# Kernel tuning notes

Hardware: AMD Instinct MI355X
Metric: run time of the kernel (lower is better)

The kernel has to match this reference:

```python
import jax, jax.numpy as jnp
import numpy as np

MAX_NUM_BINS = 200
BIN_SIZE = 500
NUM_NEIGHBORS = 5
DIST_MULT = 0.1


def setup_inputs() -> dict:
    key = jax.random.key(0)
    k1, k2 = jax.random.split(key)
    points = jax.random.normal(k1, (2, 5000, 128), dtype=jnp.float32)
    rotations = jax.random.normal(k2, (128, MAX_NUM_BINS // 2), dtype=jnp.float32)
    return {"points": points, "rotations": rotations}


def reference(points, rotations):
    # points: [B, N, D], rotations: [D, max_num_bins//2]
    B, N, D = points.shape
    nbins = N // BIN_SIZE  # module requires N % BIN_SIZE == 0

    # LSH bin assignment: project onto nbins//2 random directions, sign-split into nbins bins
    mul = jnp.einsum('bnd,dh->bnh', points, rotations[:, :nbins // 2])  # [B,N,nbins//2]
    cmul = jnp.concatenate([mul, -mul], axis=-1)                        # [B,N,nbins]
    bin_idx = jnp.argmax(cmul, axis=-1)                                 # [B,N]
    # equal-size bins via argsort of bin id (matches tf argsort+reshape)
    bins_split = jnp.argsort(bin_idx, axis=-1).reshape(B, nbins, BIN_SIZE)  # [B,nbins,S]

    # gather points per bin
    parts = jnp.take_along_axis(points, bins_split.reshape(B, N, 1), axis=1)
    parts = parts.reshape(B, nbins, BIN_SIZE, D)

    # per-bin pairwise distance -> gaussian kernel
    na = jnp.sum(parts * parts, axis=-1)                                # [B,nbins,S]
    gram = jnp.einsum('bcid,bcjd->bcij', parts, parts)                  # [B,nbins,S,S]
    dist = jnp.sqrt(jnp.maximum(na[..., :, None] - 2.0 * gram + na[..., None, :], 1e-6))
    dm = jnp.exp(-DIST_MULT * dist)                                     # [B,nbins,S,S]

    # top-k neighbors within each bin
    vals, idx = jax.lax.top_k(dm, NUM_NEIGHBORS)                        # [B,nbins,S,K]

    # map local bin indices back to global point indices
    bs_flat = bins_split.reshape(B * nbins, BIN_SIZE)
    dst = jnp.take_along_axis(bs_flat, idx.reshape(B * nbins, BIN_SIZE * NUM_NEIGHBORS), axis=1)
    dst = dst.reshape(B, nbins, BIN_SIZE, NUM_NEIGHBORS)
    src = jnp.broadcast_to(bins_split[..., None], dst.shape)
    bidx = jnp.broadcast_to(jnp.arange(B)[:, None, None, None], dst.shape)

    # scatter-add into dense [B,N,N] (sparse.add sums duplicate entries)
    out = jnp.zeros((B, N, N), dtype=points.dtype)
    out = out.at[bidx.reshape(-1), src.reshape(-1), dst.reshape(-1)].add(vals.reshape(-1))
    return out
```

## Files before the change

### kernel.cpp

```cpp
#include <hip/hip_runtime.h>
#include <cfloat>
#include <math.h>

#define NPTS   5000
#define BATCH  2
#define DIM    128
#define NBINS  10
#define BINSZ  500
#define TOPK   5
#define ROTCOLS 100

#define KB_PTS 64
#define KB_STR 129
__global__ void k_bins(const float* __restrict__ pts, const float* __restrict__ rot,
                       int* __restrict__ bin_idx, double* __restrict__ na) {
    __shared__ float P[KB_PTS * KB_STR];
    __shared__ float rotL[DIM * 5];
    int tid = threadIdx.x;
    for (int f = tid; f < DIM * 5; f += 256)
        rotL[f] = rot[(f / 5) * ROTCOLS + (f % 5)];

    int p0  = blockIdx.x * KB_PTS;
    int npb = min(KB_PTS, BATCH * NPTS - p0);

    for (int f = tid; f < npb * DIM; f += 256) {
        int r = f >> 7, d = f & 127;
        P[r * KB_STR + d] = pts[(size_t)(p0 + r) * DIM + d];
    }
    __syncthreads();

    int p = tid >> 2;
    int s = tid & 3;
    double acc[5] = {0., 0., 0., 0., 0.};
    double sq = 0.;
    const float* row = &P[p * KB_STR + s * 32];
    for (int j = 0; j < 32; ++j) {
        double v = (double)row[j];
        sq += v * v;
        int d = s * 32 + j;
#pragma unroll
        for (int h = 0; h < 5; ++h) acc[h] += v * (double)rotL[d * 5 + h];
    }
#pragma unroll
    for (int m = 1; m < 4; m <<= 1) {
#pragma unroll
        for (int h = 0; h < 5; ++h) acc[h] += __shfl_xor(acc[h], m, 4);
        sq += __shfl_xor(sq, m, 4);
    }
    if (s == 0 && p < npb) {
        double best = acc[0]; int bc = 0;
#pragma unroll
        for (int c = 1; c < NBINS; ++c) {
            double v = (c < 5) ? acc[c] : -acc[c - 5];
            if (v > best) { best = v; bc = c; }
        }
        bin_idx[p0 + p] = bc;
        na[p0 + p] = sq;
    }
}

__global__ void k_sort(const int* __restrict__ bin_idx, int* __restrict__ order) {
    const int b = blockIdx.x;
    const int t = threadIdx.x;
    const int NPT = (NPTS + 255) / 256;
    int start = t * NPT;
    int end   = min(NPTS, start + NPT);

    int cnt[NBINS];
#pragma unroll
    for (int c = 0; c < NBINS; ++c) cnt[c] = 0;
    for (int i = start; i < end; ++i) {
        int c = bin_idx[b * NPTS + i];
#pragma unroll
        for (int k = 0; k < NBINS; ++k) cnt[k] += (c == k);
    }

    __shared__ int hist[NBINS * 256];
#pragma unroll
    for (int c = 0; c < NBINS; ++c) hist[c * 256 + t] = cnt[c];
    __syncthreads();

    int base = t * NBINS;
    int s = 0;
#pragma unroll
    for (int k = 0; k < NBINS; ++k) s += hist[base + k];
    __shared__ int scan[256];
    scan[t] = s;
    __syncthreads();
    for (int off = 1; off < 256; off <<= 1) {
        int v = (t >= off) ? scan[t - off] : 0;
        __syncthreads();
        scan[t] += v;
        __syncthreads();
    }
    int run = scan[t] - s;
#pragma unroll
    for (int k = 0; k < NBINS; ++k) { int h = hist[base + k]; hist[base + k] = run; run += h; }
    __syncthreads();

    int ofs[NBINS];
#pragma unroll
    for (int c = 0; c < NBINS; ++c) ofs[c] = hist[c * 256 + t];
    for (int i = start; i < end; ++i) {
        int c = bin_idx[b * NPTS + i];
        int pos = 0;
#pragma unroll
        for (int k = 0; k < NBINS; ++k) {
            if (c == k) pos = ofs[k];
            ofs[k] += (c == k);
        }
        order[b * NPTS + pos] = i;
    }
}

#define RT    16
#define NRT   32
#define CTILE 64
#define RSTRD 130
#define CSTR  132
#define NCT   8
#define ROWQ  (NPTS/4)

__launch_bounds__(256, 3)
__global__ void k_chunks(const float* __restrict__ pts, const double* __restrict__ na,
                         const int* __restrict__ order, float* __restrict__ out) {
    __shared__ double rowPd[RT * RSTRD];
    __shared__ float  colP[CTILE * CSTR];
    __shared__ double naC[CTILE];
    __shared__ double naRs[RT];
    __shared__ int    ordR[RT];

    int blk   = blockIdx.x;
    int rt    = blk & (NRT - 1);
    int chunk = blk >> 5;
    int b     = chunk / NBINS;
    int c     = chunk % NBINS;
    int tid   = threadIdx.x;
    int row0  = rt * RT;
    int rowCount = min(RT, BINSZ - row0);

    const int*   ordBase = order + b * NPTS + c * BINSZ;
    const float* ptsB    = pts + (size_t)b * NPTS * DIM;

    for (int f = tid; f < rowCount * (DIM / 4); f += 256) {
        int r = f >> 5;
        int q = f & 31;
        int g = ordBase[row0 + r];
        float4 v = *(const float4*)(ptsB + (size_t)g * DIM + q * 4);
        double2 d01; d01.x = (double)v.x; d01.y = (double)v.y;
        double2 d23; d23.x = (double)v.z; d23.y = (double)v.w;
        *(double2*)(&rowPd[r * RSTRD + q * 4 + 0]) = d01;
        *(double2*)(&rowPd[r * RSTRD + q * 4 + 2]) = d23;
    }
    if (tid < rowCount) {
        int g = ordBase[row0 + tid];
        ordR[tid] = g;
        naRs[tid] = na[b * NPTS + g];
    }
    __syncthreads();

    int cg  = tid & 15;
    int ks  = (tid >> 4) & 1;
    int rg  = tid >> 5;
    int cgm = tid & 31;
    const int q0 = ks * 64;

    double naRr0 = (rg     < rowCount) ? naRs[rg]     : 0.;
    double naRr1 = (rg + 8 < rowCount) ? naRs[rg + 8] : 0.;

    double tv[2][TOPK];
    int    tl[2][TOPK];
#pragma unroll
    for (int ii = 0; ii < 2; ++ii)
#pragma unroll
        for (int k = 0; k < TOPK; ++k) { tv[ii][k] = DBL_MAX; tl[ii][k] = 0x7fffffff; }

    const int totalZ = rowCount * ROWQ;

    for (int ct = 0; ct < NCT; ++ct) {
        int col0T = ct * CTILE;
        int colCount = min(CTILE, BINSZ - col0T);
        __syncthreads();
        for (int f = tid; f < colCount * (DIM / 4); f += 256) {
            int j = f >> 5;
            int q = f & 31;
            int g = ordBase[col0T + j];
            float4 v = *(const float4*)(ptsB + (size_t)g * DIM + q * 4);
            *(float4*)(&colP[j * CSTR + q * 4]) = v;
        }
        if (tid < colCount) {
            int g = ordBase[col0T + tid];
            naC[tid] = na[b * NPTS + g];
        }
        __syncthreads();

        {
            float4 z = make_float4(0.f, 0.f, 0.f, 0.f);
            int z0 = (ct * totalZ) / NCT, z1 = ((ct + 1) * totalZ) / NCT;
            for (int f = z0 + tid; f < z1; f += 256) {
                int r = f / ROWQ;
                int q = f - r * ROWQ;
                float* outRow = out + ((size_t)b * NPTS + ordR[r]) * NPTS;
                *(float4*)(outRow + 4 * q) = z;
            }
        }

        double acc00 = 0., acc01 = 0., acc02 = 0., acc03 = 0.;
        double acc10 = 0., acc11 = 0., acc12 = 0., acc13 = 0.;

        for (int q = 0; q < 64; q += 4) {
            const int qq = q0 + q;
            double2 a0lo = *(const double2*)(&rowPd[rg * RSTRD + qq + 0]);
            double2 a0hi = *(const double2*)(&rowPd[rg * RSTRD + qq + 2]);
            double2 a1lo = *(const double2*)(&rowPd[(rg + 8) * RSTRD + qq + 0]);
            double2 a1hi = *(const double2*)(&rowPd[(rg + 8) * RSTRD + qq + 2]);
            float4 f0 = *(const float4*)(&colP[cg * CSTR + qq]);
            float4 f1 = *(const float4*)(&colP[(cg + 16) * CSTR + qq]);
            float4 f2 = *(const float4*)(&colP[(cg + 32) * CSTR + qq]);
            float4 f3 = *(const float4*)(&colP[(cg + 48) * CSTR + qq]);
            double b0x = (double)f0.x, b0y = (double)f0.y, b0z = (double)f0.z, b0w = (double)f0.w;
            double b1x = (double)f1.x, b1y = (double)f1.y, b1z = (double)f1.z, b1w = (double)f1.w;
            double b2x = (double)f2.x, b2y = (double)f2.y, b2z = (double)f2.z, b2w = (double)f2.w;
            double b3x = (double)f3.x, b3y = (double)f3.y, b3z = (double)f3.z, b3w = (double)f3.w;
            acc00 += a0lo.x * b0x + a0lo.y * b0y + a0hi.x * b0z + a0hi.y * b0w;
            acc01 += a0lo.x * b1x + a0lo.y * b1y + a0hi.x * b1z + a0hi.y * b1w;
            acc02 += a0lo.x * b2x + a0lo.y * b2y + a0hi.x * b2z + a0hi.y * b2w;
            acc03 += a0lo.x * b3x + a0lo.y * b3y + a0hi.x * b3z + a0hi.y * b3w;
            acc10 += a1lo.x * b0x + a1lo.y * b0y + a1hi.x * b0z + a1hi.y * b0w;
            acc11 += a1lo.x * b1x + a1lo.y * b1y + a1hi.x * b1z + a1hi.y * b1w;
            acc12 += a1lo.x * b2x + a1lo.y * b2y + a1hi.x * b2z + a1hi.y * b2w;
            acc13 += a1lo.x * b3x + a1lo.y * b3y + a1hi.x * b3z + a1hi.y * b3w;
        }

        acc00 += __shfl_xor(acc00, 16, 64);
        acc01 += __shfl_xor(acc01, 16, 64);
        acc02 += __shfl_xor(acc02, 16, 64);
        acc03 += __shfl_xor(acc03, 16, 64);
        acc10 += __shfl_xor(acc10, 16, 64);
        acc11 += __shfl_xor(acc11, 16, 64);
        acc12 += __shfl_xor(acc12, 16, 64);
        acc13 += __shfl_xor(acc13, 16, 64);

        double selA0 = ks ? acc02 : acc00;
        double selA1 = ks ? acc12 : acc10;
        double selB0 = ks ? acc03 : acc01;
        double selB1 = ks ? acc13 : acc11;
        int colA = cg + (ks ? 32 : 0);
        int colB = cg + (ks ? 48 : 16);

        if (colA < colCount) {
            int    cl = col0T + colA;
            double nc = naC[colA];
            double cv0 = fmax(naRr0 + nc - 2. * selA0, 1e-6);
            double cv1 = fmax(naRr1 + nc - 2. * selA1, 1e-6);
            int cl0 = cl, cl1 = cl;
#pragma unroll
            for (int k = 0; k < TOPK; ++k) {
                bool lt0 = (cv0 < tv[0][k]);
                double ov0 = tv[0][k]; int ol0 = tl[0][k];
                if (lt0) { tv[0][k] = cv0; tl[0][k] = cl0; cv0 = ov0; cl0 = ol0; }
                bool lt1 = (cv1 < tv[1][k]);
                double ov1 = tv[1][k]; int ol1 = tl[1][k];
                if (lt1) { tv[1][k] = cv1; tl[1][k] = cl1; cv1 = ov1; cl1 = ol1; }
            }
        }
        if (colB < colCount) {
            int    cl = col0T + colB;
            double nc = naC[colB];
            double cv0 = fmax(naRr0 + nc - 2. * selB0, 1e-6);
            double cv1 = fmax(naRr1 + nc - 2. * selB1, 1e-6);
            int cl0 = cl, cl1 = cl;
#pragma unroll
            for (int k = 0; k < TOPK; ++k) {
                bool lt0 = (cv0 < tv[0][k]);
                double ov0 = tv[0][k]; int ol0 = tl[0][k];
                if (lt0) { tv[0][k] = cv0; tl[0][k] = cl0; cv0 = ov0; cl0 = ol0; }
                bool lt1 = (cv1 < tv[1][k]);
                double ov1 = tv[1][k]; int ol1 = tl[1][k];
                if (lt1) { tv[1][k] = cv1; tl[1][k] = cl1; cv1 = ov1; cl1 = ol1; }
            }
        }
    }

#pragma unroll
    for (int m = 1; m < 32; m <<= 1) {
#pragma unroll
        for (int ii = 0; ii < 2; ++ii) {
            double rv[TOPK]; int rl[TOPK];
#pragma unroll
            for (int k = 0; k < TOPK; ++k) {
                rv[k] = __shfl_xor(tv[ii][k], m, 32);
                rl[k] = __shfl_xor(tl[ii][k], m, 32);
            }
#pragma unroll
            for (int k = 0; k < TOPK; ++k) {
                double cv = rv[k]; int cl = rl[k];
#pragma unroll
                for (int s = 0; s < TOPK; ++s) {
                    bool better = (cv < tv[ii][s]) || (cv == tv[ii][s] && cl < tl[ii][s]);
                    double ov = tv[ii][s]; int ol = tl[ii][s];
                    if (better) { tv[ii][s] = cv; tl[ii][s] = cl; cv = ov; cl = ol; }
                }
            }
        }
    }

    __syncthreads();

    if (cgm == 0) {
#pragma unroll
        for (int ii = 0; ii < 2; ++ii) {
            int r = rg + 8 * ii;
            if (r < rowCount) {
                int src = ordR[r];
                float* outRow = out + ((size_t)b * NPTS + src) * NPTS;
#pragma unroll
                for (int k = 0; k < TOPK; ++k) {
                    double dist = sqrt(tv[ii][k]);
                    double dm   = exp(-0.1 * dist);
                    int dst = ordBase[tl[ii][k]];
                    outRow[dst] = (float)dm;
                }
            }
        }
    }
}

extern "C" void kernel_launch(void* const* d_in, const int* in_sizes, int n_in,
                              void* d_out, int out_size, void* d_ws, size_t ws_size,
                              hipStream_t stream) {
    const float* pts = (const float*)d_in[0];
    const float* rot = (const float*)d_in[1];
    float* out = (float*)d_out;

    double* na      = (double*)d_ws;
    int*    bin_idx = (int*)((char*)d_ws + 80000);
    int*    order   = (int*)((char*)d_ws + 120000);

    k_bins<<<(BATCH * NPTS + KB_PTS - 1) / KB_PTS, 256, 0, stream>>>(pts, rot, bin_idx, na);
    k_sort<<<BATCH, 256, 0, stream>>>(bin_idx, order);
    k_chunks<<<BATCH * NBINS * NRT, 256, 0, stream>>>(pts, na, order, out);
}
```

Baseline: 294.5 us.

## Compute distances in fp32 with top-8 candidates, then refine top-5 in fp64

The main gram-tile loop moves from double to float arithmetic. Each row keeps 8 candidate neighbours instead of 5 so that fp32 rounding is unlikely to drop a true neighbour. Those 8 candidates are then re-scored with double-precision dot products and the final top-5 is chosen from them, which keeps the original fp64 accuracy. This replaces the slow FP64 FMAs and double-width shared memory with fp32, at the cost of a larger top-k state and an extra refinement pass that reads candidate points from global memory.

New measurement: 439.8 us. 1.49x slower.

```diff
diff --git a/kernel.cpp b/kernel.cpp
--- a/kernel.cpp
+++ b/kernel.cpp
@@ -113,22 +113,25 @@
     }
 }
 
-#define RT    16
-#define NRT   32
-#define CTILE 64
-#define RSTRD 130
-#define CSTR  132
-#define NCT   8
-#define ROWQ  (NPTS/4)
+#define RT     16
+#define NRT    32
+#define CTILE  64
+#define RSTRDF 128
+#define CSTR   132
+#define NCT    8
+#define ROWQ   (NPTS/4)
+#define TOPM   8
 
 __launch_bounds__(256, 3)
 __global__ void k_chunks(const float* __restrict__ pts, const double* __restrict__ na,
                          const int* __restrict__ order, float* __restrict__ out) {
-    __shared__ double rowPd[RT * RSTRD];
+    __shared__ float  rowPf[RT * RSTRDF];
     __shared__ float  colP[CTILE * CSTR];
-    __shared__ double naC[CTILE];
+    __shared__ float  naCf[CTILE];
     __shared__ double naRs[RT];
     __shared__ int    ordR[RT];
+    __shared__ double refVal[RT][TOPM];
+    __shared__ int    refIdx[RT][TOPM];
 
     int blk   = blockIdx.x;
     int rt    = blk & (NRT - 1);
@@ -147,10 +150,7 @@
         int q = f & 31;
         int g = ordBase[row0 + r];
         float4 v = *(const float4*)(ptsB + (size_t)g * DIM + q * 4);
-        double2 d01; d01.x = (double)v.x; d01.y = (double)v.y;
-        double2 d23; d23.x = (double)v.z; d23.y = (double)v.w;
-        *(double2*)(&rowPd[r * RSTRD + q * 4 + 0]) = d01;
-        *(double2*)(&rowPd[r * RSTRD + q * 4 + 2]) = d23;
+        *(float4*)(&rowPf[r * RSTRDF + q * 4]) = v;
     }
     if (tid < rowCount) {
         int g = ordBase[row0 + tid];
@@ -165,15 +165,15 @@
     int cgm = tid & 31;
     const int q0 = ks * 64;
 
-    double naRr0 = (rg     < rowCount) ? naRs[rg]     : 0.;
-    double naRr1 = (rg + 8 < rowCount) ? naRs[rg + 8] : 0.;
-
-    double tv[2][TOPK];
-    int    tl[2][TOPK];
+    float naRf0 = (rg     < rowCount) ? (float)naRs[rg]     : 0.f;
+    float naRf1 = (rg + 8 < rowCount) ? (float)naRs[rg + 8] : 0.f;
+
+    float tv[2][TOPM];
+    int   tl[2][TOPM];
 #pragma unroll
     for (int ii = 0; ii < 2; ++ii)
 #pragma unroll
-        for (int k = 0; k < TOPK; ++k) { tv[ii][k] = DBL_MAX; tl[ii][k] = 0x7fffffff; }
+        for (int k = 0; k < TOPM; ++k) { tv[ii][k] = FLT_MAX; tl[ii][k] = 0x7fffffff; }
 
     const int totalZ = rowCount * ROWQ;
 
@@ -190,7 +190,7 @@
         }
         if (tid < colCount) {
             int g = ordBase[col0T + tid];
-            naC[tid] = na[b * NPTS + g];
+            naCf[tid] = (float)na[b * NPTS + g];
         }
         __syncthreads();
 
@@ -205,31 +205,25 @@
             }
         }
 
-        double acc00 = 0., acc01 = 0., acc02 = 0., acc03 = 0.;
-        double acc10 = 0., acc11 = 0., acc12 = 0., acc13 = 0.;
+        float acc00 = 0.f, acc01 = 0.f, acc02 = 0.f, acc03 = 0.f;
+        float acc10 = 0.f, acc11 = 0.f, acc12 = 0.f, acc13 = 0.f;
 
         for (int q = 0; q < 64; q += 4) {
             const int qq = q0 + q;
-            double2 a0lo = *(const double2*)(&rowPd[rg * RSTRD + qq + 0]);
-            double2 a0hi = *(const double2*)(&rowPd[rg * RSTRD + qq + 2]);
-            double2 a1lo = *(const double2*)(&rowPd[(rg + 8) * RSTRD + qq + 0]);
-            double2 a1hi = *(const double2*)(&rowPd[(rg + 8) * RSTRD + qq + 2]);
+            float4 a0 = *(const float4*)(&rowPf[rg * RSTRDF + qq]);
+            float4 a1 = *(const float4*)(&rowPf[(rg + 8) * RSTRDF + qq]);
             float4 f0 = *(const float4*)(&colP[cg * CSTR + qq]);
             float4 f1 = *(const float4*)(&colP[(cg + 16) * CSTR + qq]);
             float4 f2 = *(const float4*)(&colP[(cg + 32) * CSTR + qq]);
             float4 f3 = *(const float4*)(&colP[(cg + 48) * CSTR + qq]);
-            double b0x = (double)f0.x, b0y = (double)f0.y, b0z = (double)f0.z, b0w = (double)f0.w;
-            double b1x = (double)f1.x, b1y = (double)f1.y, b1z = (double)f1.z, b1w = (double)f1.w;
-            double b2x = (double)f2.x, b2y = (double)f2.y, b2z = (double)f2.z, b2w = (double)f2.w;
-            double b3x = (double)f3.x, b3y = (double)f3.y, b3z = (double)f3.z, b3w = (double)f3.w;
-            acc00 += a0lo.x * b0x + a0lo.y * b0y + a0hi.x * b0z + a0hi.y * b0w;
-            acc01 += a0lo.x * b1x + a0lo.y * b1y + a0hi.x * b1z + a0hi.y * b1w;
-            acc02 += a0lo.x * b2x + a0lo.y * b2y + a0hi.x * b2z + a0hi.y * b2w;
-            acc03 += a0lo.x * b3x + a0lo.y * b3y + a0hi.x * b3z + a0hi.y * b3w;
-            acc10 += a1lo.x * b0x + a1lo.y * b0y + a1hi.x * b0z + a1hi.y * b0w;
-            acc11 += a1lo.x * b1x + a1lo.y * b1y + a1hi.x * b1z + a1hi.y * b1w;
-            acc12 += a1lo.x * b2x + a1lo.y * b2y + a1hi.x * b2z + a1hi.y * b2w;
-            acc13 += a1lo.x * b3x + a1lo.y * b3y + a1hi.x * b3z + a1hi.y * b3w;
+            acc00 += a0.x * f0.x + a0.y * f0.y + a0.z * f0.z + a0.w * f0.w;
+            acc01 += a0.x * f1.x + a0.y * f1.y + a0.z * f1.z + a0.w * f1.w;
+            acc02 += a0.x * f2.x + a0.y * f2.y + a0.z * f2.z + a0.w * f2.w;
+            acc03 += a0.x * f3.x + a0.y * f3.y + a0.z * f3.z + a0.w * f3.w;
+            acc10 += a1.x * f0.x + a1.y * f0.y + a1.z * f0.z + a1.w * f0.w;
+            acc11 += a1.x * f1.x + a1.y * f1.y + a1.z * f1.z + a1.w * f1.w;
+            acc12 += a1.x * f2.x + a1.y * f2.y + a1.z * f2.z + a1.w * f2.w;
+            acc13 += a1.x * f3.x + a1.y * f3.y + a1.z * f3.z + a1.w * f3.w;
         }
 
         acc00 += __shfl_xor(acc00, 16, 64);
@@ -241,42 +235,42 @@
         acc12 += __shfl_xor(acc12, 16, 64);
         acc13 += __shfl_xor(acc13, 16, 64);
 
-        double selA0 = ks ? acc02 : acc00;
-        double selA1 = ks ? acc12 : acc10;
-        double selB0 = ks ? acc03 : acc01;
-        double selB1 = ks ? acc13 : acc11;
+        float selA0 = ks ? acc02 : acc00;
+        float selA1 = ks ? acc12 : acc10;
+        float selB0 = ks ? acc03 : acc01;
+        float selB1 = ks ? acc13 : acc11;
         int colA = cg + (ks ? 32 : 0);
         int colB = cg + (ks ? 48 : 16);
 
         if (colA < colCount) {
-            int    cl = col0T + colA;
-            double nc = naC[colA];
-            double cv0 = fmax(naRr0 + nc - 2. * selA0, 1e-6);
-            double cv1 = fmax(naRr1 + nc - 2. * selA1, 1e-6);
+            int   cl = col0T + colA;
+            float nc = naCf[colA];
+            float cv0 = fmaxf(naRf0 + nc - 2.f * selA0, 1e-6f);
+            float cv1 = fmaxf(naRf1 + nc - 2.f * selA1, 1e-6f);
             int cl0 = cl, cl1 = cl;
 #pragma unroll
-            for (int k = 0; k < TOPK; ++k) {
+            for (int k = 0; k < TOPM; ++k) {
                 bool lt0 = (cv0 < tv[0][k]);
-                double ov0 = tv[0][k]; int ol0 = tl[0][k];
+                float ov0 = tv[0][k]; int ol0 = tl[0][k];
                 if (lt0) { tv[0][k] = cv0; tl[0][k] = cl0; cv0 = ov0; cl0 = ol0; }
                 bool lt1 = (cv1 < tv[1][k]);
-                double ov1 = tv[1][k]; int ol1 = tl[1][k];
+                float ov1 = tv[1][k]; int ol1 = tl[1][k];
                 if (lt1) { tv[1][k] = cv1; tl[1][k] = cl1; cv1 = ov1; cl1 = ol1; }
             }
         }
         if (colB < colCount) {
-            int    cl = col0T + colB;
-            double nc = naC[colB];
-            double cv0 = fmax(naRr0 + nc - 2. * selB0, 1e-6);
-            double cv1 = fmax(naRr1 + nc - 2. * selB1, 1e-6);
+            int   cl = col0T + colB;
+            float nc = naCf[colB];
+            float cv0 = fmaxf(naRf0 + nc - 2.f * selB0, 1e-6f);
+            float cv1 = fmaxf(naRf1 + nc - 2.f * selB1, 1e-6f);
             int cl0 = cl, cl1 = cl;
 #pragma unroll
-            for (int k = 0; k < TOPK; ++k) {
+            for (int k = 0; k < TOPM; ++k) {
                 bool lt0 = (cv0 < tv[0][k]);
-                double ov0 = tv[0][k]; int ol0 = tl[0][k];
+                float ov0 = tv[0][k]; int ol0 = tl[0][k];
                 if (lt0) { tv[0][k] = cv0; tl[0][k] = cl0; cv0 = ov0; cl0 = ol0; }
                 bool lt1 = (cv1 < tv[1][k]);
-                double ov1 = tv[1][k]; int ol1 = tl[1][k];
+                float ov1 = tv[1][k]; int ol1 = tl[1][k];
                 if (lt1) { tv[1][k] = cv1; tl[1][k] = cl1; cv1 = ov1; cl1 = ol1; }
             }
         }
@@ -286,42 +280,86 @@
     for (int m = 1; m < 32; m <<= 1) {
 #pragma unroll
         for (int ii = 0; ii < 2; ++ii) {
-            double rv[TOPK]; int rl[TOPK];
-#pragma unroll
-            for (int k = 0; k < TOPK; ++k) {
+            float rv[TOPM]; int rl[TOPM];
+#pragma unroll
+            for (int k = 0; k < TOPM; ++k) {
                 rv[k] = __shfl_xor(tv[ii][k], m, 32);
                 rl[k] = __shfl_xor(tl[ii][k], m, 32);
             }
 #pragma unroll
-            for (int k = 0; k < TOPK; ++k) {
-                double cv = rv[k]; int cl = rl[k];
-#pragma unroll
-                for (int s = 0; s < TOPK; ++s) {
+            for (int k = 0; k < TOPM; ++k) {
+                float cv = rv[k]; int cl = rl[k];
+#pragma unroll
+                for (int s = 0; s < TOPM; ++s) {
                     bool better = (cv < tv[ii][s]) || (cv == tv[ii][s] && cl < tl[ii][s]);
-                    double ov = tv[ii][s]; int ol = tl[ii][s];
+                    float ov = tv[ii][s]; int ol = tl[ii][s];
                     if (better) { tv[ii][s] = cv; tl[ii][s] = cl; cv = ov; cl = ol; }
                 }
             }
         }
     }
 
-    __syncthreads();
-
     if (cgm == 0) {
 #pragma unroll
         for (int ii = 0; ii < 2; ++ii) {
             int r = rg + 8 * ii;
-            if (r < rowCount) {
-                int src = ordR[r];
-                float* outRow = out + ((size_t)b * NPTS + src) * NPTS;
-#pragma unroll
-                for (int k = 0; k < TOPK; ++k) {
-                    double dist = sqrt(tv[ii][k]);
-                    double dm   = exp(-0.1 * dist);
-                    int dst = ordBase[tl[ii][k]];
-                    outRow[dst] = (float)dm;
-                }
-            }
+#pragma unroll
+            for (int k = 0; k < TOPM; ++k) refIdx[r][k] = tl[ii][k];
+        }
+    }
+    __syncthreads();
+
+    {
+        int u = tid >> 1;
+        int h = tid & 1;
+        int r = u >> 3;
+        int j = u & 7;
+        double dotH = 0.;
+        int cl = 0, g = 0;
+        if (r < rowCount) {
+            cl = refIdx[r][j];
+            g  = ordBase[cl];
+            const float* cp = ptsB + (size_t)g * DIM + h * 64;
+            const float* rp = &rowPf[r * RSTRDF + h * 64];
+            for (int q = 0; q < 64; q += 4) {
+                float4 cv4 = *(const float4*)(cp + q);
+                float4 rv4 = *(const float4*)(rp + q);
+                dotH += (double)rv4.x * cv4.x + (double)rv4.y * cv4.y +
+                        (double)rv4.z * cv4.z + (double)rv4.w * cv4.w;
+            }
+        }
+        double full = dotH + __shfl_xor(dotH, 1, 64);
+        if (h == 0 && r < rowCount) {
+            double naRv = naRs[r];
+            double naCv = na[b * NPTS + g];
+            refVal[r][j] = fmax(naRv + naCv - 2. * full, 1e-6);
+        }
+    }
+    __syncthreads();
+
+    if (tid < RT && tid < rowCount) {
+        double fv[TOPK]; int fl[TOPK];
+#pragma unroll
+        for (int k = 0; k < TOPK; ++k) { fv[k] = DBL_MAX; fl[k] = 0x7fffffff; }
+#pragma unroll
+        for (int j = 0; j < TOPM; ++j) {
+            double cv = refVal[tid][j];
+            int    cl = refIdx[tid][j];
+#pragma unroll
+            for (int s = 0; s < TOPK; ++s) {
+                bool better = (cv < fv[s]) || (cv == fv[s] && cl < fl[s]);
+                double ov = fv[s]; int ol = fl[s];
+                if (better) { fv[s] = cv; fl[s] = cl; cv = ov; cl = ol; }
+            }
+        }
+        int src = ordR[tid];
+        float* outRow = out + ((size_t)b * NPTS + src) * NPTS;
+#pragma unroll
+        for (int k = 0; k < TOPK; ++k) {
+            double dist = sqrt(fv[k]);
+            double dm   = exp(-0.1 * dist);
+            int dst = ordBase[fl[k]];
+            outRow[dst] = (float)dm;
         }
     }
 }
```
